# Kernel optimization log

Measured on AMD Instinct MI355X. Metric: run time of the kernel, lower is better.

The kernel has to match this reference:

```python
import jax, jax.numpy as jnp
import numpy as np

B, TQ, TK, DQ, DK = 8, 2048, 2048, 512, 512


def setup_inputs() -> dict:
    key = jax.random.key(0)
    kq, kk, kv, km, kw = jax.random.split(key, 5)
    q = jax.random.normal(kq, (B, TQ, DQ), dtype=jnp.float32)
    k = jax.random.normal(kk, (B, TK, DK), dtype=jnp.float32)
    v = jax.random.normal(kv, (B, TK, DK), dtype=jnp.float32)
    attn_mask = jax.random.randint(km, (B, TQ, TK), 0, 2) > 0
    # xavier_uniform for (DQ, DK)
    limit = float(np.sqrt(6.0 / (DQ + DK)))
    weights = jax.random.uniform(kw, (DQ, DK), minval=-limit, maxval=limit, dtype=jnp.float32)
    return {"q": q, "k": k, "v": v, "attn_mask": attn_mask, "weights": weights}


def reference(q, k, v, attn_mask, weights):
    # scores: (B, TQ, TK) = (q @ W) @ k^T
    qw = jnp.einsum('bqd,de->bqe', q, weights)
    scores = jnp.einsum('bqe,bke->bqk', qw, k)
    scores = jnp.where(attn_mask, -jnp.inf, scores)
    attention = jax.nn.softmax(scores, axis=-1)
    # dropout_rate = 0.0 -> identity
    output = jnp.einsum('bqk,bkd->bqd', attention, v)
    return (output, attention)
```

## Files before the change

### kernel.cpp

```cpp
#include <hip/hip_runtime.h>
#include <stdint.h>

#define TQs 2048
#define TKs 2048
#define DDs 512
#define NBs 8

typedef float f32x4 __attribute__((ext_vector_type(4)));
typedef float f32x2 __attribute__((ext_vector_type(2)));
typedef short bf16x8 __attribute__((ext_vector_type(8)));
typedef short bf16x4 __attribute__((ext_vector_type(4)));
typedef short bf16x2 __attribute__((ext_vector_type(2)));
typedef _Float16 half8 __attribute__((ext_vector_type(8)));

__device__ __forceinline__ unsigned short f2bf(float x){
  unsigned u = __float_as_uint(x);
  return (unsigned short)((u + 0x7fffu + ((u>>16)&1u)) >> 16);
}
__device__ __forceinline__ float bf2f(unsigned short h){
  return __uint_as_float(((unsigned)h)<<16);
}

__device__ __forceinline__ void gload16(const void* g, void* l){
  __builtin_amdgcn_global_load_lds(
      (const __attribute__((address_space(1))) unsigned int*)(unsigned long long)(uintptr_t)g,
      (__attribute__((address_space(3))) unsigned int*)(unsigned int)(uintptr_t)l,
      16, 0, 0);
}

__global__ __launch_bounds__(256) void k0_kf(const float* __restrict__ kk, _Float16* __restrict__ kf){
  const long n8 = (long)NBs*TKs*DDs/8;
  for(long i = (long)blockIdx.x*256 + threadIdx.x; i < n8; i += (long)gridDim.x*256){
    f32x4 x0 = ((const f32x4*)kk)[2*i];
    f32x4 x1 = ((const f32x4*)kk)[2*i+1];
    half8 h;
    #pragma unroll
    for(int j=0;j<4;j++){ h[j] = (_Float16)x0[j]; h[4+j] = (_Float16)x1[j]; }
    ((half8*)kf)[i] = h;
  }
}

__global__ __launch_bounds__(256) void k0_transpose_v(const float* __restrict__ v, short* __restrict__ vt){
  __shared__ float tile[64][65];
  int b = blockIdx.z;
  int t0 = blockIdx.x*64, d0 = blockIdx.y*64;
  int tid = threadIdx.x;
  int r = tid>>2, cs = (tid&3)*16;
  const float* src = v + ((long)b*TKs + t0 + r)*DDs + d0 + cs;
  #pragma unroll
  for(int i=0;i<4;i++){
    f32x4 x = ((const f32x4*)src)[i];
    tile[r][cs+4*i+0]=x[0]; tile[r][cs+4*i+1]=x[1]; tile[r][cs+4*i+2]=x[2]; tile[r][cs+4*i+3]=x[3];
  }
  __syncthreads();
  int dr = tid>>2, ts = (tid&3)*16;
  bf16x8 b0, b1;
  #pragma unroll
  for(int i=0;i<8;i++){ b0[i] = (short)f2bf(tile[ts+i][dr]); b1[i] = (short)f2bf(tile[ts+8+i][dr]); }
  short* dst = vt + ((long)b*DDs + d0 + dr)*TKs + t0 + ts;
  ((bf16x8*)dst)[0] = b0;
  ((bf16x8*)dst)[1] = b1;
}

__global__ __launch_bounds__(256) void k0_wt(const float* __restrict__ wsrc,
                                             short* __restrict__ wth, short* __restrict__ wtl){
  __shared__ float tile[64][65];
  int d0 = blockIdx.x*64, e0 = blockIdx.y*64;
  int tid = threadIdx.x;
  int r = tid>>2, cs = (tid&3)*16;
  const float* src = wsrc + ((long)(d0 + r))*DDs + e0 + cs;
  #pragma unroll
  for(int i=0;i<4;i++){
    f32x4 x = ((const f32x4*)src)[i];
    tile[r][cs+4*i+0]=x[0]; tile[r][cs+4*i+1]=x[1]; tile[r][cs+4*i+2]=x[2]; tile[r][cs+4*i+3]=x[3];
  }
  __syncthreads();
  int er = tid>>2, ds = (tid&3)*16;
  bf16x8 h0,h1,l0,l1;
  #pragma unroll
  for(int i=0;i<8;i++){
    float x = tile[ds+i][er];
    unsigned short hh = f2bf(x);
    h0[i] = (short)hh; l0[i] = (short)f2bf(x - bf2f(hh));
  }
  #pragma unroll
  for(int i=0;i<8;i++){
    float x = tile[ds+8+i][er];
    unsigned short hh = f2bf(x);
    h1[i] = (short)hh; l1[i] = (short)f2bf(x - bf2f(hh));
  }
  short* dh = wth + ((long)(e0+er))*DDs + d0 + ds;
  short* dl = wtl + ((long)(e0+er))*DDs + d0 + ds;
  ((bf16x8*)dh)[0] = h0; ((bf16x8*)dh)[1] = h1;
  ((bf16x8*)dl)[0] = l0; ((bf16x8*)dl)[1] = l1;
}

__global__ __launch_bounds__(256,2) void k1_qw(const float* __restrict__ q,
                                               const short* __restrict__ wth, const short* __restrict__ wtl,
                                               _Float16* __restrict__ qwh, _Float16* __restrict__ qwl){
  __shared__ short qah[8192], qal[8192];
  __shared__ short wbh[8192], wbl[8192];
  int q0 = blockIdx.x*128, e0 = blockIdx.y*128;
  int tid = threadIdx.x, lane = tid&63, w4 = tid>>6;
  int wm = w4>>1, wn = w4&1;
  int i15 = lane&15, g4 = lane>>4;
  f32x4 acc[4][4];
  #pragma unroll
  for(int a=0;a<4;a++)
    #pragma unroll
    for(int bq=0;bq<4;bq++) acc[a][bq] = (f32x4){0.f,0.f,0.f,0.f};
  for(int k0=0;k0<DDs;k0+=64){
    __syncthreads();
    #pragma unroll
    for(int j=0;j<4;j++){
      int J = j*4 + w4;
      long so = (long)(e0 + (J>>1)*16 + i15)*DDs + k0 + ((J&1)*4 + g4)*8;
      gload16(wth + so, &wbh[J*512]);
      gload16(wtl + so, &wbl[J*512]);
    }
    #pragma unroll
    for(int j=0;j<4;j++){
      int c = j*256 + tid;
      int ci = c&15, cg = (c>>4)&3, cks = (c>>6)&1, crb = c>>7;
      const float* s = q + (long)(q0 + crb*16 + ci)*DDs + k0 + (cks*4+cg)*8;
      f32x4 x0 = ((const f32x4*)s)[0];
      f32x4 x1 = ((const f32x4*)s)[1];
      bf16x8 h, l;
      #pragma unroll
      for(int jj=0;jj<4;jj++){
        unsigned short hj = f2bf(x0[jj]);
        h[jj] = (short)hj; l[jj] = (short)f2bf(x0[jj]-bf2f(hj));
      }
      #pragma unroll
      for(int jj=0;jj<4;jj++){
        unsigned short hj = f2bf(x1[jj]);
        h[4+jj] = (short)hj; l[4+jj] = (short)f2bf(x1[jj]-bf2f(hj));
      }
      *(bf16x8*)&qah[c*8] = h;
      *(bf16x8*)&qal[c*8] = l;
    }
    __syncthreads();
    #pragma unroll
    for(int ks=0;ks<2;ks++){
      bf16x8 a_h[4], a_l[4], b_h[4], b_l[4];
      #pragma unroll
      for(int mf=0;mf<4;mf++){
        int c = ((wm*4+mf)*2+ks)*64 + lane;
        a_h[mf] = *(const bf16x8*)&qah[c*8];
        a_l[mf] = *(const bf16x8*)&qal[c*8];
      }
      #pragma unroll
      for(int nf=0;nf<4;nf++){
        int c = ((wn*4+nf)*2+ks)*64 + lane;
        b_h[nf] = *(const bf16x8*)&wbh[c*8];
        b_l[nf] = *(const bf16x8*)&wbl[c*8];
      }
      #pragma unroll
      for(int mf=0;mf<4;mf++)
      #pragma unroll
      for(int nf=0;nf<4;nf++){
        acc[mf][nf] = __builtin_amdgcn_mfma_f32_16x16x32_bf16(a_h[mf], b_h[nf], acc[mf][nf],0,0,0);
        acc[mf][nf] = __builtin_amdgcn_mfma_f32_16x16x32_bf16(a_h[mf], b_l[nf], acc[mf][nf],0,0,0);
        acc[mf][nf] = __builtin_amdgcn_mfma_f32_16x16x32_bf16(a_l[mf], b_h[nf], acc[mf][nf],0,0,0);
      }
    }
  }
  int rr = g4*4, cc = i15;
  #pragma unroll
  for(int mf=0;mf<4;mf++)
  #pragma unroll
  for(int nf=0;nf<4;nf++)
  #pragma unroll
  for(int r2=0;r2<4;r2++){
    long row = q0 + wm*64 + mf*16 + rr + r2;
    long col = e0 + wn*64 + nf*16 + cc;
    float s = acc[mf][nf][r2];
    _Float16 h = (_Float16)s;
    qwh[row*DDs + col] = h;
    qwl[row*DDs + col] = (_Float16)(s - (float)h);
  }
}

__global__ __launch_bounds__(256,2) void k2a(const _Float16* __restrict__ qwh, const _Float16* __restrict__ qwl,
                                             const _Float16* __restrict__ kf,
                                             const int* __restrict__ mask, float* __restrict__ attn,
                                             float* __restrict__ m_ws, float* __restrict__ l_ws){
  __shared__ _Float16 kb[2][16384];
  int rb = blockIdx.x;
  int chunk = blockIdx.y;
  int tid = threadIdx.x, lane = tid&63, w = tid>>6;
  int b = rb>>5;
  long qrow0 = (long)rb*64 + w*16;
  int i15 = lane&15, g4 = lane>>4;
  half8 ah[16], al[16];
  {
    const _Float16* ph = qwh + (qrow0 + i15)*DDs + g4*8;
    const _Float16* pl = qwl + (qrow0 + i15)*DDs + g4*8;
    #pragma unroll
    for(int kc=0;kc<16;kc++){
      ah[kc] = *(const half8*)(ph + kc*32);
      al[kc] = *(const half8*)(pl + kc*32);
    }
  }
  float m_st[4], l_st[4];
  #pragma unroll
  for(int r=0;r<4;r++){ m_st[r]=-1e30f; l_st[r]=0.f; }
  const _Float16* kbase = kf + (long)b*TKs*DDs;
  int mv_pf[2][4];
  {
    int t0 = chunk*1024;
    #pragma unroll
    for(int j=0;j<8;j++){
      int J = j*4 + w;
      long so = (long)(t0 + ((J>>4)<<4) + i15)*DDs + (J&15)*32 + g4*8;
      gload16(kbase + so, &kb[0][J*512]);
    }
    #pragma unroll
    for(int nf=0;nf<2;nf++)
      #pragma unroll
      for(int r=0;r<4;r++)
        mv_pf[nf][r] = mask[(qrow0 + g4*4 + r)*TKs + t0 + nf*16 + i15];
  }
  __syncthreads();
  int cur = 0;
  for(int it=0; it<32; ++it){
    int t0 = chunk*1024 + it*32;
    if(it < 31){
      int t1 = t0 + 32;
      #pragma unroll
      for(int j=0;j<8;j++){
        int J = j*4 + w;
        long so = (long)(t1 + ((J>>4)<<4) + i15)*DDs + (J&15)*32 + g4*8;
        gload16(kbase + so, &kb[cur^1][J*512]);
      }
    }
    int mv[2][4];
    #pragma unroll
    for(int nf=0;nf<2;nf++)
      #pragma unroll
      for(int r=0;r<4;r++)
        mv[nf][r] = mv_pf[nf][r];
    if(it < 31){
      int t1 = t0 + 32;
      #pragma unroll
      for(int nf=0;nf<2;nf++)
        #pragma unroll
        for(int r=0;r<4;r++)
          mv_pf[nf][r] = mask[(qrow0 + g4*4 + r)*TKs + t1 + nf*16 + i15];
    }
    f32x4 acc[2];
    acc[0]=(f32x4){0.f,0.f,0.f,0.f}; acc[1]=(f32x4){0.f,0.f,0.f,0.f};
    #pragma unroll
    for(int ks=0;ks<16;ks++){
      #pragma unroll
      for(int nf=0;nf<2;nf++){
        half8 bh = *(const half8*)&kb[cur][((nf*16+ks)*64 + lane)*8];
        acc[nf] = __builtin_amdgcn_mfma_f32_16x16x32_f16(ah[ks], bh, acc[nf],0,0,0);
        acc[nf] = __builtin_amdgcn_mfma_f32_16x16x32_f16(al[ks], bh, acc[nf],0,0,0);
      }
    }
    #pragma unroll
    for(int r=0;r<4;r++){
      float s0 = acc[0][r];
      float s1 = acc[1][r];
      if(mv[0][r]) s0 = -3e38f;
      if(mv[1][r]) s1 = -3e38f;
      float mo = m_st[r];
      float mn = fmaxf(mo, fmaxf(s0,s1));
      l_st[r] = l_st[r]*__expf(mo-mn) + __expf(s0-mn) + __expf(s1-mn);
      m_st[r] = mn;
      long row = qrow0 + g4*4 + r;
      attn[row*TKs + t0 + i15] = s0;
      attn[row*TKs + t0 + 16 + i15] = s1;
    }
    __syncthreads();
    cur ^= 1;
  }
  #pragma unroll
  for(int r=0;r<4;r++){
    #pragma unroll
    for(int d=1; d<16; d<<=1){
      float m2 = __shfl_xor(m_st[r], d, 16);
      float l2 = __shfl_xor(l_st[r], d, 16);
      float mn = fmaxf(m_st[r], m2);
      l_st[r] = l_st[r]*__expf(m_st[r]-mn) + l2*__expf(m2-mn);
      m_st[r] = mn;
    }
  }
  if(i15==0){
    #pragma unroll
    for(int r=0;r<4;r++){
      long row = qrow0 + g4*4 + r;
      m_ws[row*2 + chunk] = m_st[r];
      l_ws[row*2 + chunk] = l_st[r];
    }
  }
}

__global__ __launch_bounds__(512,4) void k2b(const short* __restrict__ vt, const float* __restrict__ m_ws,
                                             const float* __restrict__ l_ws, float* __restrict__ attn,
                                             float* __restrict__ outp){
  __shared__ short vf[2][16384];
  __shared__ short at2[2][1024];
  __shared__ float ms[32], rls[32];
  int rb = blockIdx.x;
  long row0 = (long)rb*32;
  int b = rb>>6;
  int tid=threadIdx.x, lane=tid&63, w=tid>>6;
  int i15 = lane&15, g4 = lane>>4;
  const short* vb = vt + (long)b*DDs*TKs;
  float* arow = attn + row0*TKs;
  int r_n = ((tid>>8)<<4) | (lane>>2);
  int tn  = (((tid>>6)&3)<<3) | ((lane&3)<<1);
  int nbyte = ((tid>>6)<<8) | (lane<<2);
  #pragma unroll
  for(int j=0;j<4;j++){
    int J = j*8 + w;
    long so = (long)(J*16 + i15)*TKs + g4*8;
    gload16(vb + so, &vf[0][J*512]);
  }
  f32x2 s_pf = *(const f32x2*)(arow + (long)r_n*TKs + tn);
  if(tid < 32){
    long row = row0 + tid;
    float m0=m_ws[row*2+0], m1=m_ws[row*2+1];
    float M = fmaxf(m0,m1);
    float L = l_ws[row*2+0]*__expf(m0-M) + l_ws[row*2+1]*__expf(m1-M);
    ms[tid] = M;
    rls[tid] = 1.0f/L;
  }
  __syncthreads();
  {
    float M = ms[r_n], RL = rls[r_n];
    float a0 = __expf(s_pf[0]-M)*RL, a1 = __expf(s_pf[1]-M)*RL;
    f32x2 av; av[0]=a0; av[1]=a1;
    *(f32x2*)(arow + (long)r_n*TKs + tn) = av;
    bf16x2 ab; ab[0]=(short)f2bf(a0); ab[1]=(short)f2bf(a1);
    *(bf16x2*)((char*)at2[0] + nbyte) = ab;
  }
  s_pf = *(const f32x2*)(arow + (long)r_n*TKs + 32 + tn);
  __syncthreads();
  f32x4 acc[2][4];
  #pragma unroll
  for(int mf=0;mf<2;mf++)
    #pragma unroll
    for(int nf=0;nf<4;nf++) acc[mf][nf]=(f32x4){0.f,0.f,0.f,0.f};
  int c = 0;
  for(int it=0; it<64; ++it){
    if(it < 63){
      int t1 = (it+1)*32;
      #pragma unroll
      for(int j=0;j<4;j++){
        int J = j*8 + w;
        long so = (long)(J*16 + i15)*TKs + t1 + g4*8;
        gload16(vb + so, &vf[c^1][J*512]);
      }
    }
    f32x2 s_cur = s_pf;
    if(it < 62)
      s_pf = *(const f32x2*)(arow + (long)r_n*TKs + (it+2)*32 + tn);
    bf16x8 af[2], bfr[4];
    #pragma unroll
    for(int mf=0;mf<2;mf++) af[mf] = *(const bf16x8*)&at2[c][(mf*64 + lane)*8];
    #pragma unroll
    for(int nf=0;nf<4;nf++) bfr[nf] = *(const bf16x8*)&vf[c][((w*4+nf)*64 + lane)*8];
    #pragma unroll
    for(int mf=0;mf<2;mf++)
    #pragma unroll
    for(int nf=0;nf<4;nf++)
      acc[mf][nf] = __builtin_amdgcn_mfma_f32_16x16x32_bf16(af[mf], bfr[nf], acc[mf][nf],0,0,0);
    if(it < 63){
      int t1 = (it+1)*32;
      float M = ms[r_n], RL = rls[r_n];
      float a0 = __expf(s_cur[0]-M)*RL, a1 = __expf(s_cur[1]-M)*RL;
      f32x2 av; av[0]=a0; av[1]=a1;
      *(f32x2*)(arow + (long)r_n*TKs + t1 + tn) = av;
      bf16x2 ab; ab[0]=(short)f2bf(a0); ab[1]=(short)f2bf(a1);
      *(bf16x2*)((char*)at2[c^1] + nbyte) = ab;
    }
    __syncthreads();
    c ^= 1;
  }
  #pragma unroll
  for(int mf=0;mf<2;mf++)
  #pragma unroll
  for(int nf=0;nf<4;nf++)
  #pragma unroll
  for(int r2=0;r2<4;r2++){
    long row = row0 + mf*16 + g4*4 + r2;
    long col = w*64 + nf*16 + i15;
    outp[row*DDs + col] = acc[mf][nf][r2];
  }
}

extern "C" void kernel_launch(void* const* d_in, const int* in_sizes, int n_in,
                              void* d_out, int out_size, void* d_ws, size_t ws_size,
                              hipStream_t stream) {
  const float* q    = (const float*)d_in[0];
  const float* k    = (const float*)d_in[1];
  const float* v    = (const float*)d_in[2];
  const int*   mask = (const int*)d_in[3];
  const float* wsrc = (const float*)d_in[4];
  float* outp = (float*)d_out;
  float* attn = (float*)d_out + (long)NBs*TQs*DDs;
  char* ws = (char*)d_ws;
  const long NE = (long)NBs*TKs*DDs;
  _Float16* kf  = (_Float16*)ws;
  short*    vt  = (short*)(ws + 2*NE);
  _Float16* qwh = (_Float16*)(ws + 4*NE);
  _Float16* qwl = (_Float16*)(ws + 6*NE);
  float* m_ws = (float*)(ws + 8*NE);
  float* l_ws = (float*)(ws + 8*NE + 65536*4);
  short* wth = (short*)attn;
  short* wtl = (short*)attn + 262144;
  hipLaunchKernelGGL(k0_kf,          dim3(1024),    dim3(256), 0, stream, k, kf);
  hipLaunchKernelGGL(k0_transpose_v, dim3(32,8,8),  dim3(256), 0, stream, v, vt);
  hipLaunchKernelGGL(k0_wt,          dim3(8,8),     dim3(256), 0, stream, wsrc, wth, wtl);
  hipLaunchKernelGGL(k1_qw,          dim3(128,4),   dim3(256), 0, stream, q, wth, wtl, qwh, qwl);
  hipLaunchKernelGGL(k2a,            dim3(256,2),   dim3(256), 0, stream, qwh, qwl, kf, mask, attn, m_ws, l_ws);
  hipLaunchKernelGGL(k2b,            dim3(512),     dim3(512), 0, stream, vt, m_ws, l_ws, attn, outp);
}
```

Measured before the change: 349.1 us.

## Bit-pack mask, split PV into single-wave tiles and separate softmax normalize pass

Adds a pre-pass that packs the int mask into 64-bit ballot words, so the score kernel reads bits instead of a full int per element. The PV kernel is rebuilt as 64-thread blocks that each handle a 32-row by 128-column output tile, loading scores and transposed V straight from global memory into registers with no LDS or barriers. Normalized attention is then written back by a separate streaming kernel. In exchange, the extra pass re-reads the full mask once, the raw scores are now read twice (once by PV, once by normalize), and each PV block recomputes the exponentials for its column slice.

```diff
diff --git a/kernel.cpp b/kernel.cpp
--- a/kernel.cpp
+++ b/kernel.cpp
@@ -10,7 +10,6 @@
 typedef float f32x2 __attribute__((ext_vector_type(2)));
 typedef short bf16x8 __attribute__((ext_vector_type(8)));
 typedef short bf16x4 __attribute__((ext_vector_type(4)));
-typedef short bf16x2 __attribute__((ext_vector_type(2)));
 typedef _Float16 half8 __attribute__((ext_vector_type(8)));
 
 __device__ __forceinline__ unsigned short f2bf(float x){
@@ -37,6 +36,16 @@
     #pragma unroll
     for(int j=0;j<4;j++){ h[j] = (_Float16)x0[j]; h[4+j] = (_Float16)x1[j]; }
     ((half8*)kf)[i] = h;
+  }
+}
+
+__global__ __launch_bounds__(256) void k0_mb(const int* __restrict__ mask, unsigned long long* __restrict__ mbits){
+  const long n = (long)NBs*TQs*TKs;
+  int lane = threadIdx.x & 63;
+  for(long i = (long)blockIdx.x*256 + threadIdx.x; i < n; i += (long)gridDim.x*256){
+    int v = mask[i];
+    unsigned long long bal = __ballot(v != 0);
+    if(lane == 0) mbits[i>>6] = bal;
   }
 }
 
@@ -183,7 +192,8 @@
 
 __global__ __launch_bounds__(256,2) void k2a(const _Float16* __restrict__ qwh, const _Float16* __restrict__ qwl,
                                              const _Float16* __restrict__ kf,
-                                             const int* __restrict__ mask, float* __restrict__ attn,
+                                             const unsigned long long* __restrict__ mbits,
+                                             float* __restrict__ attn,
                                              float* __restrict__ m_ws, float* __restrict__ l_ws){
   __shared__ _Float16 kb[2][16384];
   int rb = blockIdx.x;
@@ -206,7 +216,7 @@
   #pragma unroll
   for(int r=0;r<4;r++){ m_st[r]=-1e30f; l_st[r]=0.f; }
   const _Float16* kbase = kf + (long)b*TKs*DDs;
-  int mv_pf[2][4];
+  unsigned long long wb_pf[4];
   {
     int t0 = chunk*1024;
     #pragma unroll
@@ -216,10 +226,8 @@
       gload16(kbase + so, &kb[0][J*512]);
     }
     #pragma unroll
-    for(int nf=0;nf<2;nf++)
-      #pragma unroll
-      for(int r=0;r<4;r++)
-        mv_pf[nf][r] = mask[(qrow0 + g4*4 + r)*TKs + t0 + nf*16 + i15];
+    for(int r=0;r<4;r++)
+      wb_pf[r] = mbits[(qrow0 + g4*4 + r)*(TKs/64) + (t0>>6)];
   }
   __syncthreads();
   int cur = 0;
@@ -234,19 +242,14 @@
         gload16(kbase + so, &kb[cur^1][J*512]);
       }
     }
-    int mv[2][4];
-    #pragma unroll
-    for(int nf=0;nf<2;nf++)
-      #pragma unroll
-      for(int r=0;r<4;r++)
-        mv[nf][r] = mv_pf[nf][r];
+    unsigned long long wb[4];
+    #pragma unroll
+    for(int r=0;r<4;r++) wb[r] = wb_pf[r];
     if(it < 31){
       int t1 = t0 + 32;
       #pragma unroll
-      for(int nf=0;nf<2;nf++)
-        #pragma unroll
-        for(int r=0;r<4;r++)
-          mv_pf[nf][r] = mask[(qrow0 + g4*4 + r)*TKs + t1 + nf*16 + i15];
+      for(int r=0;r<4;r++)
+        wb_pf[r] = mbits[(qrow0 + g4*4 + r)*(TKs/64) + (t1>>6)];
     }
     f32x4 acc[2];
     acc[0]=(f32x4){0.f,0.f,0.f,0.f}; acc[1]=(f32x4){0.f,0.f,0.f,0.f};
@@ -259,12 +262,13 @@
         acc[nf] = __builtin_amdgcn_mfma_f32_16x16x32_f16(al[ks], bh, acc[nf],0,0,0);
       }
     }
+    int hsh = (t0 & 32);
     #pragma unroll
     for(int r=0;r<4;r++){
       float s0 = acc[0][r];
       float s1 = acc[1][r];
-      if(mv[0][r]) s0 = -3e38f;
-      if(mv[1][r]) s1 = -3e38f;
+      if((wb[r] >> (hsh + i15)) & 1ULL) s0 = -3e38f;
+      if((wb[r] >> (hsh + 16 + i15)) & 1ULL) s1 = -3e38f;
       float mo = m_st[r];
       float mn = fmaxf(mo, fmaxf(s0,s1));
       l_st[r] = l_st[r]*__expf(mo-mn) + __expf(s0-mn) + __expf(s1-mn);
@@ -297,98 +301,97 @@
   }
 }
 
-__global__ __launch_bounds__(512,4) void k2b(const short* __restrict__ vt, const float* __restrict__ m_ws,
-                                             const float* __restrict__ l_ws, float* __restrict__ attn,
-                                             float* __restrict__ outp){
-  __shared__ short vf[2][16384];
-  __shared__ short at2[2][1024];
-  __shared__ float ms[32], rls[32];
-  int rb = blockIdx.x;
-  long row0 = (long)rb*32;
-  int b = rb>>6;
-  int tid=threadIdx.x, lane=tid&63, w=tid>>6;
-  int i15 = lane&15, g4 = lane>>4;
-  const short* vb = vt + (long)b*DDs*TKs;
-  float* arow = attn + row0*TKs;
-  int r_n = ((tid>>8)<<4) | (lane>>2);
-  int tn  = (((tid>>6)&3)<<3) | ((lane&3)<<1);
-  int nbyte = ((tid>>6)<<8) | (lane<<2);
-  #pragma unroll
-  for(int j=0;j<4;j++){
-    int J = j*8 + w;
-    long so = (long)(J*16 + i15)*TKs + g4*8;
-    gload16(vb + so, &vf[0][J*512]);
-  }
-  f32x2 s_pf = *(const f32x2*)(arow + (long)r_n*TKs + tn);
-  if(tid < 32){
-    long row = row0 + tid;
-    float m0=m_ws[row*2+0], m1=m_ws[row*2+1];
-    float M = fmaxf(m0,m1);
+__global__ __launch_bounds__(64,2) void k2b(const short* __restrict__ vt, const float* __restrict__ m_ws,
+                                            const float* __restrict__ l_ws, const float* __restrict__ attn,
+                                            float* __restrict__ outp){
+  int bid = blockIdx.x;
+  int b  = bid >> 8;
+  int rg = (bid >> 2) & 63;
+  int dg = bid & 3;
+  long row0 = (long)b*TQs + rg*32;
+  int dv0 = dg*128;
+  int lane = threadIdx.x;
+  int i15 = lane & 15, g4 = lane >> 4;
+  float M[2], RL[2];
+  #pragma unroll
+  for(int mf=0; mf<2; mf++){
+    long row = row0 + mf*16 + i15;
+    float m0 = m_ws[row*2+0], m1 = m_ws[row*2+1];
+    float Mm = fmaxf(m0, m1);
+    float L = l_ws[row*2+0]*__expf(m0-Mm) + l_ws[row*2+1]*__expf(m1-Mm);
+    M[mf] = Mm; RL[mf] = 1.0f/L;
+  }
+  const float* sp0 = attn + (row0 + i15)*TKs + g4*8;
+  const float* sp1 = attn + (row0 + 16 + i15)*TKs + g4*8;
+  const short* vp = vt + ((long)b*DDs + dv0 + i15)*TKs + g4*8;
+  f32x4 sn00 = ((const f32x4*)sp0)[0], sn01 = ((const f32x4*)sp0)[1];
+  f32x4 sn10 = ((const f32x4*)sp1)[0], sn11 = ((const f32x4*)sp1)[1];
+  bf16x8 bvn[8];
+  #pragma unroll
+  for(int nf=0;nf<8;nf++)
+    bvn[nf] = *(const bf16x8*)(vp + (long)nf*16*TKs);
+  f32x4 acc[2][8];
+  #pragma unroll
+  for(int mf=0;mf<2;mf++)
+    #pragma unroll
+    for(int nf=0;nf<8;nf++) acc[mf][nf] = (f32x4){0.f,0.f,0.f,0.f};
+  for(int it=0; it<64; ++it){
+    int t0 = it*32;
+    f32x4 sc00 = sn00, sc01 = sn01, sc10 = sn10, sc11 = sn11;
+    bf16x8 bv[8];
+    #pragma unroll
+    for(int nf=0;nf<8;nf++) bv[nf] = bvn[nf];
+    if(it < 63){
+      sn00 = *(const f32x4*)(sp0 + t0 + 32);
+      sn01 = *(const f32x4*)(sp0 + t0 + 36);
+      sn10 = *(const f32x4*)(sp1 + t0 + 32);
+      sn11 = *(const f32x4*)(sp1 + t0 + 36);
+      #pragma unroll
+      for(int nf=0;nf<8;nf++)
+        bvn[nf] = *(const bf16x8*)(vp + (long)nf*16*TKs + t0 + 32);
+    }
+    bf16x8 pf[2];
+    #pragma unroll
+    for(int mf=0;mf<2;mf++){
+      f32x4 s0 = mf ? sc10 : sc00;
+      f32x4 s1 = mf ? sc11 : sc01;
+      bf16x8 p;
+      #pragma unroll
+      for(int j=0;j<4;j++){
+        p[j]   = (short)f2bf(__expf(s0[j]-M[mf])*RL[mf]);
+        p[4+j] = (short)f2bf(__expf(s1[j]-M[mf])*RL[mf]);
+      }
+      pf[mf] = p;
+    }
+    #pragma unroll
+    for(int mf=0;mf<2;mf++)
+      #pragma unroll
+      for(int nf=0;nf<8;nf++)
+        acc[mf][nf] = __builtin_amdgcn_mfma_f32_16x16x32_bf16(pf[mf], bv[nf], acc[mf][nf],0,0,0);
+  }
+  #pragma unroll
+  for(int mf=0;mf<2;mf++)
+  #pragma unroll
+  for(int nf=0;nf<8;nf++)
+  #pragma unroll
+  for(int r=0;r<4;r++)
+    outp[(row0 + mf*16 + g4*4 + r)*DDs + dv0 + nf*16 + i15] = acc[mf][nf][r];
+}
+
+__global__ __launch_bounds__(256) void k2c(const float* __restrict__ m_ws, const float* __restrict__ l_ws,
+                                           float* __restrict__ attn){
+  const long nv = (long)NBs*TQs*TKs/4;
+  for(long i = (long)blockIdx.x*256 + threadIdx.x; i < nv; i += (long)gridDim.x*256){
+    long row = i >> 9;
+    float m0 = m_ws[row*2+0], m1 = m_ws[row*2+1];
+    float M = fmaxf(m0, m1);
     float L = l_ws[row*2+0]*__expf(m0-M) + l_ws[row*2+1]*__expf(m1-M);
-    ms[tid] = M;
-    rls[tid] = 1.0f/L;
-  }
-  __syncthreads();
-  {
-    float M = ms[r_n], RL = rls[r_n];
-    float a0 = __expf(s_pf[0]-M)*RL, a1 = __expf(s_pf[1]-M)*RL;
-    f32x2 av; av[0]=a0; av[1]=a1;
-    *(f32x2*)(arow + (long)r_n*TKs + tn) = av;
-    bf16x2 ab; ab[0]=(short)f2bf(a0); ab[1]=(short)f2bf(a1);
-    *(bf16x2*)((char*)at2[0] + nbyte) = ab;
-  }
-  s_pf = *(const f32x2*)(arow + (long)r_n*TKs + 32 + tn);
-  __syncthreads();
-  f32x4 acc[2][4];
-  #pragma unroll
-  for(int mf=0;mf<2;mf++)
-    #pragma unroll
-    for(int nf=0;nf<4;nf++) acc[mf][nf]=(f32x4){0.f,0.f,0.f,0.f};
-  int c = 0;
-  for(int it=0; it<64; ++it){
-    if(it < 63){
-      int t1 = (it+1)*32;
-      #pragma unroll
-      for(int j=0;j<4;j++){
-        int J = j*8 + w;
-        long so = (long)(J*16 + i15)*TKs + t1 + g4*8;
-        gload16(vb + so, &vf[c^1][J*512]);
-      }
-    }
-    f32x2 s_cur = s_pf;
-    if(it < 62)
-      s_pf = *(const f32x2*)(arow + (long)r_n*TKs + (it+2)*32 + tn);
-    bf16x8 af[2], bfr[4];
-    #pragma unroll
-    for(int mf=0;mf<2;mf++) af[mf] = *(const bf16x8*)&at2[c][(mf*64 + lane)*8];
-    #pragma unroll
-    for(int nf=0;nf<4;nf++) bfr[nf] = *(const bf16x8*)&vf[c][((w*4+nf)*64 + lane)*8];
-    #pragma unroll
-    for(int mf=0;mf<2;mf++)
-    #pragma unroll
-    for(int nf=0;nf<4;nf++)
-      acc[mf][nf] = __builtin_amdgcn_mfma_f32_16x16x32_bf16(af[mf], bfr[nf], acc[mf][nf],0,0,0);
-    if(it < 63){
-      int t1 = (it+1)*32;
-      float M = ms[r_n], RL = rls[r_n];
-      float a0 = __expf(s_cur[0]-M)*RL, a1 = __expf(s_cur[1]-M)*RL;
-      f32x2 av; av[0]=a0; av[1]=a1;
-      *(f32x2*)(arow + (long)r_n*TKs + t1 + tn) = av;
-      bf16x2 ab; ab[0]=(short)f2bf(a0); ab[1]=(short)f2bf(a1);
-      *(bf16x2*)((char*)at2[c^1] + nbyte) = ab;
-    }
-    __syncthreads();
-    c ^= 1;
-  }
-  #pragma unroll
-  for(int mf=0;mf<2;mf++)
-  #pragma unroll
-  for(int nf=0;nf<4;nf++)
-  #pragma unroll
-  for(int r2=0;r2<4;r2++){
-    long row = row0 + mf*16 + g4*4 + r2;
-    long col = w*64 + nf*16 + i15;
-    outp[row*DDs + col] = acc[mf][nf][r2];
+    float RL = 1.0f/L;
+    f32x4 s = ((const f32x4*)attn)[i];
+    f32x4 a;
+    #pragma unroll
+    for(int j=0;j<4;j++) a[j] = __expf(s[j]-M)*RL;
+    ((f32x4*)attn)[i] = a;
   }
 }
 
@@ -410,12 +413,15 @@
   _Float16* qwl = (_Float16*)(ws + 6*NE);
   float* m_ws = (float*)(ws + 8*NE);
   float* l_ws = (float*)(ws + 8*NE + 65536*4);
+  unsigned long long* mbits = (unsigned long long*)(ws + 8*NE + 1048576);
   short* wth = (short*)attn;
   short* wtl = (short*)attn + 262144;
   hipLaunchKernelGGL(k0_kf,          dim3(1024),    dim3(256), 0, stream, k, kf);
+  hipLaunchKernelGGL(k0_mb,          dim3(2048),    dim3(256), 0, stream, mask, mbits);
   hipLaunchKernelGGL(k0_transpose_v, dim3(32,8,8),  dim3(256), 0, stream, v, vt);
   hipLaunchKernelGGL(k0_wt,          dim3(8,8),     dim3(256), 0, stream, wsrc, wth, wtl);
   hipLaunchKernelGGL(k1_qw,          dim3(128,4),   dim3(256), 0, stream, q, wth, wtl, qwh, qwl);
-  hipLaunchKernelGGL(k2a,            dim3(256,2),   dim3(256), 0, stream, qwh, qwl, kf, mask, attn, m_ws, l_ws);
-  hipLaunchKernelGGL(k2b,            dim3(512),     dim3(512), 0, stream, vt, m_ws, l_ws, attn, outp);
-}
+  hipLaunchKernelGGL(k2a,            dim3(256,2),   dim3(256), 0, stream, qwh, qwl, kf, mbits, attn, m_ws, l_ws);
+  hipLaunchKernelGGL(k2b,            dim3(2048),    dim3(64),  0, stream, vt, m_ws, l_ws, attn, outp);
+  hipLaunchKernelGGL(k2c,            dim3(2048),    dim3(256), 0, stream, m_ws, l_ws, attn);
+}
```

After: 438.8 us. +25.7%, slower.
